# Kernel optimization log

Measured on AMD Instinct MI355X. Metric: run time of the kernel, lower is better.

Reference implementation:

```python
import jax, jax.numpy as jnp
import numpy as np

N = 4096
IN_SIZE = 512
MLP_W = 16
HID = 512
MID = 64  # hardcoded tgc2 output size in the torch module
OUT = 128
BN_EPS = 1e-5


def setup_inputs() -> dict:
    key = jax.random.key(0)
    ks = jax.random.split(key, 24)
    adj = (jax.random.uniform(ks[0], (N, N)) < 0.05).astype(jnp.float32)
    xdeg = jax.random.uniform(ks[1], (N, N), dtype=jnp.float32)
    ydeg = jax.random.uniform(ks[2], (N, N), dtype=jnp.float32)
    u = lambda k, sh, fan: jax.random.uniform(k, sh, jnp.float32, -1.0, 1.0) / np.sqrt(fan)
    return {
        "adj": adj, "xdeg": xdeg, "ydeg": ydeg,
        # edge MLP: 3 -> MLP_W -> 2
        "mlp_w1": u(ks[3], (3, MLP_W), 3), "mlp_b1": jnp.zeros((MLP_W,), jnp.float32),
        "mlp_w2": u(ks[4], (MLP_W, 2), MLP_W), "mlp_b2": jnp.zeros((2,), jnp.float32),
        # positional linear: Linear(N, in_size) applied to eye(N) -> pe = W^T + b
        "pe_w": u(ks[5], (N, IN_SIZE), N), "pe_b": jnp.zeros((IN_SIZE,), jnp.float32),
        # GCN weights
        "gc1_w": u(ks[6], (IN_SIZE, HID), HID),
        "lin2_w": u(ks[7], (HID, MID), HID), "lin2_b": jnp.zeros((MID,), jnp.float32),
        "gc3_w": u(ks[8], (MID, OUT), OUT),
        # BatchNorm (eval mode: running stats)
        "bn1_g": jnp.ones((HID,), jnp.float32), "bn1_b": jnp.zeros((HID,), jnp.float32),
        "bn1_m": jnp.zeros((HID,), jnp.float32), "bn1_v": jnp.ones((HID,), jnp.float32),
        "bn2_g": jnp.ones((OUT,), jnp.float32), "bn2_b": jnp.zeros((OUT,), jnp.float32),
        "bn2_m": jnp.zeros((OUT,), jnp.float32), "bn2_v": jnp.ones((OUT,), jnp.float32),
    }


def reference(adj, xdeg, ydeg, mlp_w1, mlp_b1, mlp_w2, mlp_b2, pe_w, pe_b,
              gc1_w, lin2_w, lin2_b, gc3_w,
              bn1_g, bn1_b, bn1_m, bn1_v, bn2_g, bn2_b, bn2_m, bn2_v):
    # Edge MLP + softmax over [adj, xdeg, ydeg] features; torch only computes it
    # at nonzero adj entries then scatters into a dense mask. Since the mask is
    # multiplied by adj, computing densely and multiplying is exactly equivalent.
    feats = jnp.stack([adj, xdeg, ydeg], axis=-1)          # [N, N, 3]
    h = jax.nn.relu(jnp.einsum('nmf,fw->nmw', feats, mlp_w1) + mlp_b1)
    logits = jnp.einsum('nmw,wc->nmc', h, mlp_w2) + mlp_b2  # [N, N, 2]
    mask = jax.nn.softmax(logits, axis=-1)[..., 1]          # [N, N]
    a = adj * mask + jnp.eye(adj.shape[0], dtype=adj.dtype)

    # Degree normalization: A' = D_row^{-1/2} A D_col^{-1/2} (broadcast, no diag matmuls)
    rowsum = jnp.sum(a, axis=1)
    colsum = jnp.sum(a, axis=0)
    d_row = jnp.where(rowsum > 0, rowsum ** -0.5, 0.0)
    d_col = jnp.where(colsum > 0, colsum ** -0.5, 0.0)
    a = d_row[:, None] * a * d_col[None, :]

    # pe = Linear(eye(N)) = W^T + b (eval mode, dropout off)
    pe = pe_w + pe_b[None, :]                               # [N, IN_SIZE]

    h = a @ (pe @ gc1_w)                                    # GCN layer 1
    h = (h - bn1_m) * (bn1_g / jnp.sqrt(bn1_v + BN_EPS)) + bn1_b
    h = h @ lin2_w + lin2_b                                 # tgc2
    mid = h
    h = jax.nn.relu(h)
    h = a @ (h @ gc3_w)                                     # GCN layer 3
    out = (h - bn2_m) * (bn2_g / jnp.sqrt(bn2_v + BN_EPS)) + bn2_b
    return out, mid
```

## Files before the change

### kernel.cpp

```cpp
#include <hip/hip_runtime.h>
#include <hip/hip_bf16.h>

#define NN 4096
#define INS 512
#define HIDW 512
#define MIDW 64
#define OUTW 128
#define CAP 384
#define SEG 96
#define BN_EPS 1e-5f
#define NSTRIP 8
#define NPAIR (NSTRIP / 2)
#define SLOTCAP (NSTRIP * SEG)
#define CS_BLOCKS 256
#define CS_ROWS 16

__device__ __forceinline__ void thin_block(
    const float* __restrict__ A, const float* __restrict__ B,
    const float* __restrict__ abias, float* __restrict__ C, int K, int bb,
    float (*As)[36], float (*Bs)[64])
{
    const int t = threadIdx.x;
    const int bm = bb * 32;
    const int c2 = t & 31, rg = t >> 5;

    float acc[4][2] = {};
    for (int k0 = 0; k0 < K; k0 += 64) {
        float va[8];
        #pragma unroll
        for (int l = 0; l < 8; ++l) {
            int e = t + l * 256;
            va[l] = A[(size_t)(bm + (e >> 6)) * K + k0 + (e & 63)];
        }
        float vb[16];
        #pragma unroll
        for (int l = 0; l < 16; ++l) {
            int e = t + l * 256;
            vb[l] = B[(size_t)(k0 + (e >> 6)) * 64 + (e & 63)];
        }
        #pragma unroll
        for (int l = 0; l < 8; ++l) {
            int e = t + l * 256;
            float v = va[l];
            if (abias) v += abias[k0 + (e & 63)];
            As[e & 63][e >> 6] = v;
        }
        #pragma unroll
        for (int l = 0; l < 16; ++l) {
            int e = t + l * 256;
            Bs[e >> 6][e & 63] = vb[l];
        }
        __syncthreads();
        #pragma unroll
        for (int k = 0; k < 64; ++k) {
            float4 a4 = *reinterpret_cast<const float4*>(&As[k][rg * 4]);
            float2 b2 = *reinterpret_cast<const float2*>(&Bs[k][2 * c2]);
            acc[0][0] = fmaf(a4.x, b2.x, acc[0][0]);
            acc[0][1] = fmaf(a4.x, b2.y, acc[0][1]);
            acc[1][0] = fmaf(a4.y, b2.x, acc[1][0]);
            acc[1][1] = fmaf(a4.y, b2.y, acc[1][1]);
            acc[2][0] = fmaf(a4.z, b2.x, acc[2][0]);
            acc[2][1] = fmaf(a4.z, b2.y, acc[2][1]);
            acc[3][0] = fmaf(a4.w, b2.x, acc[3][0]);
            acc[3][1] = fmaf(a4.w, b2.y, acc[3][1]);
        }
        __syncthreads();
    }
    #pragma unroll
    for (int u = 0; u < 4; ++u) {
        int r = bm + rg * 4 + u;
        *reinterpret_cast<float2*>(&C[(size_t)r * 64 + 2 * c2]) =
            make_float2(acc[u][0], acc[u][1]);
    }
}

__global__ __launch_bounds__(256) void k_count_prep(
    const float* __restrict__ adj,
    int* __restrict__ cslot, int* __restrict__ cnt, int* __restrict__ dflag,
    const float* __restrict__ lin2_w, const float* __restrict__ lin2_b,
    const float* __restrict__ bn1_g, const float* __restrict__ bn1_b,
    const float* __restrict__ bn1_m, const float* __restrict__ bn1_v,
    const float* __restrict__ bn2_g, const float* __restrict__ bn2_b,
    const float* __restrict__ bn2_m, const float* __restrict__ bn2_v,
    float* __restrict__ Wp, float* __restrict__ c1,
    float* __restrict__ s2g, float* __restrict__ t2g)
{
    const int t = threadIdx.x;
    if (blockIdx.x == 0) {
        __shared__ float t1s[HIDW];
        for (int h = t; h < HIDW; h += 256) {
            float s1 = bn1_g[h] * rsqrtf(bn1_v[h] + BN_EPS);
            t1s[h] = bn1_b[h] - bn1_m[h] * s1;
            for (int m = 0; m < MIDW; ++m)
                Wp[(size_t)h * MIDW + m] = s1 * lin2_w[(size_t)h * MIDW + m];
        }
        __syncthreads();
        if (t < MIDW) {
            float acc = lin2_b[t];
            for (int h = 0; h < HIDW; ++h)
                acc = fmaf(t1s[h], lin2_w[(size_t)h * MIDW + t], acc);
            c1[t] = acc;
        } else if (t >= 64 && t < 64 + OUTW) {
            int j = t - 64;
            float s2 = bn2_g[j] * rsqrtf(bn2_v[j] + BN_EPS);
            s2g[j] = s2;
            t2g[j] = bn2_b[j] - bn2_m[j] * s2;
        }
        return;
    }
    const int wave = t >> 6, lane = t & 63;
    const int gw = (blockIdx.x - 1) * 4 + wave;
    const int i = gw >> 3, s = gw & 7;
    const int colbase = s * 512;
    const float* __restrict__ base = adj + (size_t)i * NN + colbase + 4 * lane;
    float4 a4a = *reinterpret_cast<const float4*>(base);
    float4 a4b = *reinterpret_cast<const float4*>(base + 256);
    const float av[8] = {a4a.x, a4a.y, a4a.z, a4a.w,
                         a4b.x, a4b.y, a4b.z, a4b.w};
    int* __restrict__ slot = cslot + (size_t)i * SLOTCAP + s * SEG;
    const unsigned long long lt = (1ULL << lane) - 1ULL;
    int run = 0;
    #pragma unroll
    for (int c = 0; c < 8; ++c) {
        int col = colbase + ((c < 4) ? (4 * lane + c) : (256 + 4 * lane + c - 4));
        bool diag = (col == i);
        bool act = (av[c] != 0.f) || diag;
        if (diag) dflag[i] = (av[c] != 0.f) ? 1 : 0;
        unsigned long long m = __ballot(act);
        if (act) {
            int pos = run + __popcll(m & lt);
            if (pos < SEG) slot[pos] = col;
        }
        run += __popcll(m);
    }
    if (lane == 0) cnt[gw] = (run < SEG) ? run : SEG;
}

__global__ __launch_bounds__(256) void k_fill_w2(
    const float* __restrict__ xdeg, const float* __restrict__ ydeg,
    const int* __restrict__ cslot, const int* __restrict__ cnt,
    const int* __restrict__ dflag,
    const float* __restrict__ w1, const float* __restrict__ b1,
    const float* __restrict__ w2, const float* __restrict__ b2,
    float* __restrict__ a_vals, int* __restrict__ a_cols,
    float* __restrict__ rs_part,
    const float* __restrict__ gc1_w, const float* __restrict__ Wp,
    float* __restrict__ W2)
{
    __shared__ float As[64][36];
    __shared__ float Bs[64][64];
    if (blockIdx.x < INS / 32) {
        thin_block(gc1_w, Wp, nullptr, W2, HIDW, blockIdx.x, As, Bs);
        return;
    }
    __shared__ float shb[16], sw1x[16], sw1y[16], sw2[32], sb2[2];
    const int t = threadIdx.x;
    const int wave = t >> 6, lane = t & 63;
    if (t < 16) {
        shb[t]  = b1[t] + w1[t];
        sw1x[t] = w1[16 + t];
        sw1y[t] = w1[32 + t];
    }
    if (t < 32) sw2[t] = w2[t];
    if (t < 2)  sb2[t] = b2[t];
    __syncthreads();

    const int q = __builtin_amdgcn_readfirstlane(
        (blockIdx.x - INS / 32) * 4 + wave);
    const int i = q >> 2;
    const int sp = (q & 3) * 2;
    const int* __restrict__ cb = cnt + i * NSTRIP;
    int wb = 0;
    #pragma unroll
    for (int ss = 0; ss < NSTRIP; ++ss) if (ss < sp) wb += cb[ss];
    const int n0 = cb[sp];
    const int ntot = n0 + cb[sp + 1];
    const int hasde = dflag[i];
    const int* __restrict__ slot = cslot + (size_t)i * SLOTCAP + sp * SEG;
    const float* __restrict__ xrow = xdeg + (size_t)i * NN;
    const float* __restrict__ yrow = ydeg + (size_t)i * NN;
    float* __restrict__ gv = a_vals + (size_t)i * CAP;
    int*   __restrict__ gc = a_cols + (size_t)i * CAP;

    float local = 0.f;
    for (int p = lane; p < ntot; p += 64) {
        int col = (p < n0) ? slot[p] : slot[SEG + p - n0];
        float x = xrow[col];
        float y = yrow[col];
        float l0 = sb2[0], l1 = sb2[1];
        #pragma unroll
        for (int w = 0; w < 16; ++w) {
            float hw = fmaf(x, sw1x[w], shb[w]);
            hw = fmaf(y, sw1y[w], hw);
            hw = fmaxf(hw, 0.f);
            l0 = fmaf(hw, sw2[2 * w],     l0);
            l1 = fmaf(hw, sw2[2 * w + 1], l1);
        }
        float v = 1.f / (1.f + __expf(l0 - l1));
        if (col == i) v = hasde ? (v + 1.f) : 1.f;
        int gp = wb + p;
        if (gp < CAP) { gc[gp] = col; gv[gp] = v; }
        local += v;
    }
    #pragma unroll
    for (int o = 32; o >= 1; o >>= 1)
        local += __shfl_down(local, o, 64);
    if (lane == 0) rs_part[q] = local;
}

__global__ __launch_bounds__(256) void k_thin_g(
    const float* __restrict__ pe_w, const float* __restrict__ pe_b,
    const float* __restrict__ W2, float* __restrict__ G)
{
    __shared__ float As[64][36];
    __shared__ float Bs[64][64];
    thin_block(pe_w, W2, pe_b, G, INS, blockIdx.x, As, Bs);
}

__global__ __launch_bounds__(256) void k_colsum(
    const float* __restrict__ a_vals, const int* __restrict__ a_cols,
    const int* __restrict__ cnt, float* __restrict__ P)
{
    __shared__ float ls[NN];
    const int t = threadIdx.x;
    const int wave = t >> 6, lane = t & 63;
    const int b = blockIdx.x;
    for (int j = t; j < NN; j += 256) ls[j] = 0.f;
    __syncthreads();
    const int r0 = b * CS_ROWS;
    #pragma unroll
    for (int rr = 0; rr < 4; ++rr) {
        const int r = r0 + wave * 4 + rr;
        int n = 0;
        #pragma unroll
        for (int ss = 0; ss < NSTRIP; ++ss) n += cnt[r * NSTRIP + ss];
        n = (n < CAP) ? n : CAP;
        const float* __restrict__ vr = a_vals + (size_t)r * CAP;
        const int*   __restrict__ cr = a_cols + (size_t)r * CAP;
        for (int p0 = 4 * lane; p0 < n; p0 += 256) {
            float4 v4 = *reinterpret_cast<const float4*>(vr + p0);
            int4   c4 = *reinterpret_cast<const int4*>(cr + p0);
            if (p0 + 0 < n) atomicAdd(&ls[c4.x], v4.x);
            if (p0 + 1 < n) atomicAdd(&ls[c4.y], v4.y);
            if (p0 + 2 < n) atomicAdd(&ls[c4.z], v4.z);
            if (p0 + 3 < n) atomicAdd(&ls[c4.w], v4.w);
        }
    }
    __syncthreads();
    for (int j = t; j < NN; j += 256)
        P[(size_t)b * NN + j] = ls[j];
}

__global__ __launch_bounds__(512) void k_scale(
    const float* __restrict__ rs_part, const float* __restrict__ P,
    float* __restrict__ d_row, float* __restrict__ d_col)
{
    int j = blockIdx.x * 512 + threadIdx.x;
    float r = 0.f;
    #pragma unroll
    for (int s = 0; s < NPAIR; ++s) r += rs_part[j * NPAIR + s];
    d_row[j] = (r > 0.f) ? 1.f / sqrtf(r) : 0.f;
    float c = 0.f;
    for (int b = 0; b < CS_BLOCKS; ++b)
        c += P[(size_t)b * NN + j];
    d_col[j] = (c > 0.f) ? 1.f / sqrtf(c) : 0.f;
}

template <bool WITH_MID>
__global__ __launch_bounds__(256) void k_spmm(
    const float* __restrict__ a_vals, const int* __restrict__ a_cols,
    const int* __restrict__ cnt, const float* __restrict__ X,
    const float* __restrict__ d_row, const float* __restrict__ d_col,
    const float* __restrict__ c1,
    const float* __restrict__ gc3, const float* __restrict__ s2g,
    const float* __restrict__ t2g,
    float* __restrict__ O1, float* __restrict__ O2)
{
    __shared__ float sv[2][CAP];
    __shared__ int   scl[2][CAP];
    __shared__ float sacc[4][64];
    const int t = threadIdx.x;
    const int wave = t >> 6, lane = t & 63;
    const int rb = wave >> 1, h = wave & 1;
    const int i = blockIdx.x * 2 + rb;
    int n = 0;
    #pragma unroll
    for (int ss = 0; ss < NSTRIP; ++ss) n += cnt[i * NSTRIP + ss];
    n = (n < CAP) ? n : CAP;
    const int n16 = (n + 15) & ~15;
    const float* __restrict__ vrow = a_vals + (size_t)i * CAP;
    const int*   __restrict__ crow = a_cols + (size_t)i * CAP;

    for (int p = h * 64 + lane; p < n16; p += 128) {
        bool ok = p < n;
        int c = ok ? crow[p] : 0;
        float v = ok ? vrow[p] : 0.f;
        if (WITH_MID) v *= d_col[c];
        sv[rb][p]  = v;
        scl[rb][p] = c;
    }
    __syncthreads();

    const int eh = lane >> 5;
    const int lc = lane & 31;
    const int Q  = n16 >> 1;
    const int Qh = Q >> 1;

    float a0 = 0.f, a1 = 0.f;
    for (int q = h * Qh; q < (h + 1) * Qh; q += 4) {
        #pragma unroll
        for (int j = 0; j < 4; ++j) {
            int p = 2 * (q + j) + eh;
            float v = sv[rb][p];
            int c = scl[rb][p];
            float2 x = *reinterpret_cast<const float2*>(X + (size_t)c * 64 + 2 * lc);
            a0 = fmaf(v, x.x, a0);
            a1 = fmaf(v, x.y, a1);
        }
    }
    a0 += __shfl_xor(a0, 32);
    a1 += __shfl_xor(a1, 32);
    if (lane < 32) { sacc[wave][2 * lc] = a0; sacc[wave][2 * lc + 1] = a1; }
    __syncthreads();

    if (WITH_MID) {
        if (h == 0 && lane < 32) {
            float s0 = sacc[wave][2 * lc]     + sacc[wave + 1][2 * lc];
            float s1 = sacc[wave][2 * lc + 1] + sacc[wave + 1][2 * lc + 1];
            float dr = d_row[i];
            float dc = d_col[i];
            float m0 = fmaf(s0, dr, c1[2 * lc]);
            float m1 = fmaf(s1, dr, c1[2 * lc + 1]);
            *reinterpret_cast<float2*>(O1 + (size_t)i * 64 + 2 * lc) =
                make_float2(m0, m1);
            *reinterpret_cast<float2*>(O2 + (size_t)i * 64 + 2 * lc) =
                make_float2(dc * fmaxf(m0, 0.f), dc * fmaxf(m1, 0.f));
        }
    } else {
        if (h == 0 && lane < 32) {
            float dr = d_row[i];
            float s0 = (sacc[wave][2 * lc]     + sacc[wave + 1][2 * lc])     * dr;
            float s1 = (sacc[wave][2 * lc + 1] + sacc[wave + 1][2 * lc + 1]) * dr;
            sacc[wave][2 * lc]     = s0;
            sacc[wave][2 * lc + 1] = s1;
        }
        __syncthreads();
        const int rb2 = t >> 7;
        const int j = t & 127;
        const float* __restrict__ srow = sacc[2 * rb2];
        float acc = 0.f;
        #pragma unroll 8
        for (int k = 0; k < 64; ++k)
            acc = fmaf(srow[k], gc3[k * 128 + j], acc);
        int orow = blockIdx.x * 2 + rb2;
        O1[(size_t)orow * 128 + j] = fmaf(acc, s2g[j], t2g[j]);
    }
}

extern "C" void kernel_launch(void* const* d_in, const int* in_sizes, int n_in,
                              void* d_out, int out_size, void* d_ws, size_t ws_size,
                              hipStream_t stream) {
    const float* adj    = (const float*)d_in[0];
    const float* xdeg   = (const float*)d_in[1];
    const float* ydeg   = (const float*)d_in[2];
    const float* mlp_w1 = (const float*)d_in[3];
    const float* mlp_b1 = (const float*)d_in[4];
    const float* mlp_w2 = (const float*)d_in[5];
    const float* mlp_b2 = (const float*)d_in[6];
    const float* pe_w   = (const float*)d_in[7];
    const float* pe_b   = (const float*)d_in[8];
    const float* gc1_w  = (const float*)d_in[9];
    const float* lin2_w = (const float*)d_in[10];
    const float* lin2_b = (const float*)d_in[11];
    const float* gc3_w  = (const float*)d_in[12];
    const float* bn1_g  = (const float*)d_in[13];
    const float* bn1_b  = (const float*)d_in[14];
    const float* bn1_m  = (const float*)d_in[15];
    const float* bn1_v  = (const float*)d_in[16];
    const float* bn2_g  = (const float*)d_in[17];
    const float* bn2_b  = (const float*)d_in[18];
    const float* bn2_m  = (const float*)d_in[19];
    const float* bn2_v  = (const float*)d_in[20];

    float* out = (float*)d_out;
    float* mid = out + (size_t)NN * OUTW;

    char* w = (char*)d_ws;
    float* a_vals = (float*)w;  w += (size_t)NN * CAP * 4;
    int*   a_cols = (int*)w;    w += (size_t)NN * CAP * 4;
    int*   cslot  = (int*)w;    w += (size_t)NN * SLOTCAP * 4;
    int*   cnt    = (int*)w;    w += (size_t)NN * NSTRIP * 4;
    int*   dflag  = (int*)w;    w += (size_t)NN * 4;
    float* rs_part= (float*)w;  w += (size_t)NN * NPAIR * 4;
    float* d_row  = (float*)w;  w += (size_t)NN * 4;
    float* d_col  = (float*)w;  w += (size_t)NN * 4;
    float* P      = (float*)w;  w += (size_t)CS_BLOCKS * NN * 4;
    float* Wp     = (float*)w;  w += (size_t)HIDW * MIDW * 4;
    float* W2     = (float*)w;  w += (size_t)INS * MIDW * 4;
    float* c1     = (float*)w;  w += 256;
    float* s2g    = (float*)w;  w += 512;
    float* t2g    = (float*)w;  w += 512;
    float* G      = (float*)w;  w += (size_t)NN * MIDW * 4;
    float* R      = (float*)w;  w += (size_t)NN * MIDW * 4;

    k_count_prep<<<NN * NSTRIP / 4 + 1, 256, 0, stream>>>(
        adj, cslot, cnt, dflag, lin2_w, lin2_b, bn1_g, bn1_b, bn1_m, bn1_v,
        bn2_g, bn2_b, bn2_m, bn2_v, Wp, c1, s2g, t2g);
    k_fill_w2<<<INS / 32 + NN * NPAIR / 4, 256, 0, stream>>>(
        xdeg, ydeg, cslot, cnt, dflag, mlp_w1, mlp_b1, mlp_w2, mlp_b2,
        a_vals, a_cols, rs_part, gc1_w, Wp, W2);
    k_thin_g<<<NN / 32, 256, 0, stream>>>(pe_w, pe_b, W2, G);
    k_colsum<<<CS_BLOCKS, 256, 0, stream>>>(a_vals, a_cols, cnt, P);
    k_scale<<<NN / 512, 512, 0, stream>>>(rs_part, P, d_row, d_col);
    k_spmm<true><<<NN / 2, 256, 0, stream>>>(
        a_vals, a_cols, cnt, G, d_row, d_col, c1,
        nullptr, nullptr, nullptr, mid, R);
    k_spmm<false><<<NN / 2, 256, 0, stream>>>(
        a_vals, a_cols, cnt, R, d_row, d_col, nullptr,
        gc3_w, s2g, t2g, out, nullptr);
}
```

Baseline: 122.8 us.

## Fold BN1 scaling into W2 GEMM and merge G GEMM into fill kernel

The BN1 scale is now applied on the fly when the lin2 weights are loaded into shared memory, so the separate Wp precompute loop is gone. The gc1_w·lin2' product (W2) now runs as extra blocks of the adjacency-count kernel. The pe·W2 thin GEMM (G) runs as extra blocks of the edge-MLP fill kernel. This removes one kernel launch and one dependency stage by co-scheduling independent work. In exchange, both fused kernels carry more shared memory, and each B tile load now does extra rsqrt work.

```diff
diff --git a/kernel.cpp b/kernel.cpp
--- a/kernel.cpp
+++ b/kernel.cpp
@@ -15,9 +15,12 @@
 #define CS_BLOCKS 256
 #define CS_ROWS 16
 
+template <bool BSCALE>
 __device__ __forceinline__ void thin_block(
     const float* __restrict__ A, const float* __restrict__ B,
-    const float* __restrict__ abias, float* __restrict__ C, int K, int bb,
+    const float* __restrict__ abias,
+    const float* __restrict__ bg, const float* __restrict__ bv,
+    float* __restrict__ C, int K, int bb,
     float (*As)[36], float (*Bs)[64])
 {
     const int t = threadIdx.x;
@@ -48,7 +51,12 @@
         #pragma unroll
         for (int l = 0; l < 16; ++l) {
             int e = t + l * 256;
-            Bs[e >> 6][e & 63] = vb[l];
+            float v = vb[l];
+            if (BSCALE) {
+                int k = k0 + (e >> 6);
+                v *= bg[k] * rsqrtf(bv[k] + BN_EPS);
+            }
+            Bs[e >> 6][e & 63] = v;
         }
         __syncthreads();
         #pragma unroll
@@ -77,12 +85,13 @@
 __global__ __launch_bounds__(256) void k_count_prep(
     const float* __restrict__ adj,
     int* __restrict__ cslot, int* __restrict__ cnt, int* __restrict__ dflag,
+    const float* __restrict__ gc1_w,
     const float* __restrict__ lin2_w, const float* __restrict__ lin2_b,
     const float* __restrict__ bn1_g, const float* __restrict__ bn1_b,
     const float* __restrict__ bn1_m, const float* __restrict__ bn1_v,
     const float* __restrict__ bn2_g, const float* __restrict__ bn2_b,
     const float* __restrict__ bn2_m, const float* __restrict__ bn2_v,
-    float* __restrict__ Wp, float* __restrict__ c1,
+    float* __restrict__ W2, float* __restrict__ c1,
     float* __restrict__ s2g, float* __restrict__ t2g)
 {
     const int t = threadIdx.x;
@@ -91,8 +100,6 @@
         for (int h = t; h < HIDW; h += 256) {
             float s1 = bn1_g[h] * rsqrtf(bn1_v[h] + BN_EPS);
             t1s[h] = bn1_b[h] - bn1_m[h] * s1;
-            for (int m = 0; m < MIDW; ++m)
-                Wp[(size_t)h * MIDW + m] = s1 * lin2_w[(size_t)h * MIDW + m];
         }
         __syncthreads();
         if (t < MIDW) {
@@ -108,8 +115,15 @@
         }
         return;
     }
+    if (blockIdx.x <= INS / 32) {
+        __shared__ float As[64][36];
+        __shared__ float Bs[64][64];
+        thin_block<true>(gc1_w, lin2_w, nullptr, bn1_g, bn1_v, W2, HIDW,
+                         blockIdx.x - 1, As, Bs);
+        return;
+    }
     const int wave = t >> 6, lane = t & 63;
-    const int gw = (blockIdx.x - 1) * 4 + wave;
+    const int gw = (blockIdx.x - 1 - INS / 32) * 4 + wave;
     const int i = gw >> 3, s = gw & 7;
     const int colbase = s * 512;
     const float* __restrict__ base = adj + (size_t)i * NN + colbase + 4 * lane;
@@ -136,7 +150,7 @@
     if (lane == 0) cnt[gw] = (run < SEG) ? run : SEG;
 }
 
-__global__ __launch_bounds__(256) void k_fill_w2(
+__global__ __launch_bounds__(256) void k_fill_g(
     const float* __restrict__ xdeg, const float* __restrict__ ydeg,
     const int* __restrict__ cslot, const int* __restrict__ cnt,
     const int* __restrict__ dflag,
@@ -144,13 +158,14 @@
     const float* __restrict__ w2, const float* __restrict__ b2,
     float* __restrict__ a_vals, int* __restrict__ a_cols,
     float* __restrict__ rs_part,
-    const float* __restrict__ gc1_w, const float* __restrict__ Wp,
-    float* __restrict__ W2)
+    const float* __restrict__ pe_w, const float* __restrict__ pe_b,
+    const float* __restrict__ W2, float* __restrict__ G)
 {
     __shared__ float As[64][36];
     __shared__ float Bs[64][64];
-    if (blockIdx.x < INS / 32) {
-        thin_block(gc1_w, Wp, nullptr, W2, HIDW, blockIdx.x, As, Bs);
+    if (blockIdx.x < NN / 32) {
+        thin_block<false>(pe_w, W2, pe_b, nullptr, nullptr, G, INS,
+                          blockIdx.x, As, Bs);
         return;
     }
     __shared__ float shb[16], sw1x[16], sw1y[16], sw2[32], sb2[2];
@@ -166,7 +181,7 @@
     __syncthreads();
 
     const int q = __builtin_amdgcn_readfirstlane(
-        (blockIdx.x - INS / 32) * 4 + wave);
+        (blockIdx.x - NN / 32) * 4 + wave);
     const int i = q >> 2;
     const int sp = (q & 3) * 2;
     const int* __restrict__ cb = cnt + i * NSTRIP;
@@ -206,15 +221,6 @@
     for (int o = 32; o >= 1; o >>= 1)
         local += __shfl_down(local, o, 64);
     if (lane == 0) rs_part[q] = local;
-}
-
-__global__ __launch_bounds__(256) void k_thin_g(
-    const float* __restrict__ pe_w, const float* __restrict__ pe_b,
-    const float* __restrict__ W2, float* __restrict__ G)
-{
-    __shared__ float As[64][36];
-    __shared__ float Bs[64][64];
-    thin_block(pe_w, W2, pe_b, G, INS, blockIdx.x, As, Bs);
 }
 
 __global__ __launch_bounds__(256) void k_colsum(
@@ -395,7 +401,6 @@
     float* d_row  = (float*)w;  w += (size_t)NN * 4;
     float* d_col  = (float*)w;  w += (size_t)NN * 4;
     float* P      = (float*)w;  w += (size_t)CS_BLOCKS * NN * 4;
-    float* Wp     = (float*)w;  w += (size_t)HIDW * MIDW * 4;
     float* W2     = (float*)w;  w += (size_t)INS * MIDW * 4;
     float* c1     = (float*)w;  w += 256;
     float* s2g    = (float*)w;  w += 512;
@@ -403,13 +408,13 @@
     float* G      = (float*)w;  w += (size_t)NN * MIDW * 4;
     float* R      = (float*)w;  w += (size_t)NN * MIDW * 4;
 
-    k_count_prep<<<NN * NSTRIP / 4 + 1, 256, 0, stream>>>(
-        adj, cslot, cnt, dflag, lin2_w, lin2_b, bn1_g, bn1_b, bn1_m, bn1_v,
-        bn2_g, bn2_b, bn2_m, bn2_v, Wp, c1, s2g, t2g);
-    k_fill_w2<<<INS / 32 + NN * NPAIR / 4, 256, 0, stream>>>(
+    k_count_prep<<<1 + INS / 32 + NN * NSTRIP / 4, 256, 0, stream>>>(
+        adj, cslot, cnt, dflag, gc1_w, lin2_w, lin2_b,
+        bn1_g, bn1_b, bn1_m, bn1_v, bn2_g, bn2_b, bn2_m, bn2_v,
+        W2, c1, s2g, t2g);
+    k_fill_g<<<NN / 32 + NN * NPAIR / 4, 256, 0, stream>>>(
         xdeg, ydeg, cslot, cnt, dflag, mlp_w1, mlp_b1, mlp_w2, mlp_b2,
-        a_vals, a_cols, rs_part, gc1_w, Wp, W2);
-    k_thin_g<<<NN / 32, 256, 0, stream>>>(pe_w, pe_b, W2, G);
+        a_vals, a_cols, rs_part, pe_w, pe_b, W2, G);
     k_colsum<<<CS_BLOCKS, 256, 0, stream>>>(a_vals, a_cols, cnt, P);
     k_scale<<<NN / 512, 512, 0, stream>>>(rs_part, P, d_row, d_col);
     k_spmm<true><<<NN / 2, 256, 0, stream>>>(
```

Measured after the change: 131.8 us. +7.3%, slower.
